# Kernel tuning notes

Measured on AMD Instinct MI355X. Metric: run time of the kernel, lower is better.

Reference implementation:

```python
import jax, jax.numpy as jnp
import numpy as np

B, N, D, R, NUM_HEADS, S = 8, 512, 256, 6, 3, 1000


def setup_inputs() -> dict:
    key = jax.random.key(0)
    ks = jax.random.split(key, 12)
    init = lambda k, shape: jax.random.normal(k, shape, jnp.float32) * 0.02
    return {
        "symbol_ids": jax.random.randint(ks[0], (B, N), 0, S),
        "positions": jax.random.normal(ks[1], (B, N, 2), jnp.float32),
        "sym_table": init(ks[2], (S, D)),
        "layer_table": init(ks[3], (S, D)),      # layer-0 interpretation embedding
        "rel_W": init(ks[4], (R, D, D)),          # per-relation Linear weights (in,out)
        "rel_b": init(ks[5], (R, D)),
        "h1_W": init(ks[6], (NUM_HEADS, D, D)),   # interpretation head Linear1
        "h1_b": init(ks[7], (NUM_HEADS, D)),
        "h2_W": init(ks[8], (NUM_HEADS, D)),      # interpretation head Linear2 (D->1)
        "h2_b": init(ks[9], (NUM_HEADS,)),
        "out_W": init(ks[10], (D, D)),
        "out_b": init(ks[11], (D,)),
    }


def _relation_type(dx, dy):
    # Vectorized version of PositionalGrammar._get_relation_type (if/elif chain)
    return jnp.select(
        [dy > 0.5, dy < -0.5, dx < -0.5, dx > 0.5,
         (jnp.abs(dx) < 0.3) & (jnp.abs(dy) < 0.3)],
        [0, 1, 2, 3, 4], 5)


def _positional_grammar(symbols, positions, rel_W, rel_b):
    # transformed[b,j] = symbols[b,j] + sum_{i!=j} (symbols[b,i] @ W_r(i,j) + b_r(i,j))
    dx = positions[:, None, :, 0] - positions[:, :, None, 0]  # [b,i,j]
    dy = positions[:, None, :, 1] - positions[:, :, None, 1]
    rel = _relation_type(dx, dy)                               # [b,i,j] int
    n = symbols.shape[1]
    not_self = ~jnp.eye(n, dtype=bool)
    # one-hot relation mask, self-pairs excluded: [b,i,j,r]
    M = ((rel[..., None] == jnp.arange(R)) & not_self[None, :, :, None]).astype(symbols.dtype)
    T = jnp.einsum('bid,rde->brie', symbols, rel_W)            # per-relation transform of sources
    contrib = jnp.einsum('bijr,brie->bje', M, T)               # scatter-add over sources i
    bias = jnp.einsum('bijr,re->bje', M, rel_b)                # per-pair bias accumulation
    return symbols + contrib + bias


def reference(symbol_ids, positions, sym_table, layer_table, rel_W, rel_b,
              h1_W, h1_b, h2_W, h2_b, out_W, out_b):
    # SymbolEmbedding (calendar_pos=None path; layer=0)
    symbols = sym_table[symbol_ids] + layer_table[symbol_ids]  # [B,N,D]
    # PositionalGrammar
    symbols = _positional_grammar(symbols, positions, rel_W, rel_b)
    # LayeredInterpretation: 3 heads of Linear-GELU-Linear(D->1)
    h = jax.nn.gelu(jnp.einsum('bnd,rde->brne', symbols, h1_W)
                    + h1_b[None, :, None, :], approximate=False)
    interp = jnp.einsum('brne,re->brn', h, h2_W) + h2_b[None, :, None]  # [B,3,N]
    # output projection
    output = symbols @ out_W + out_b
    return (output,
            interp[:, 0, :, None],   # exoteric  [B,N,1]
            interp[:, 1, :, None],   # esoteric
            interp[:, 2, :, None],   # sacred
            symbols)
```

## Files before the change

kernel.cpp:

```cpp
#include <hip/hip_runtime.h>
#include <hip/hip_bf16.h>
#include <math.h>

#define BB 8
#define NN 512
#define DD 256
#define BNT 4096

typedef __attribute__((ext_vector_type(8))) short short8;
typedef __attribute__((ext_vector_type(4))) float f32x4;

#define OFF_S0T   0u
#define OFF_GC    524288u
#define OFF_WCT   3670016u
#define OFF_WBT   3866624u
#define OFF_BB    3997696u
#define OFF_CNT   3998720u
#define OFF_REL   4015104u

#define OUT0_OFF   0u
#define INTERP_OFF 1048576u
#define SYM_OFF    1060864u

__device__ __forceinline__ float gelu_exact(float x) {
    return 0.5f * x * (1.0f + erff(x * 0.70710678118654752f));
}

__device__ __forceinline__ ushort f2bf(float x) {
    __hip_bfloat16 h = __float2bfloat16(x);
    union { __hip_bfloat16 b; ushort u; } cv;
    cv.b = h;
    return cv.u;
}

typedef __attribute__((address_space(3))) unsigned int  lds_u32;
typedef __attribute__((address_space(1))) unsigned int  glb_u32;
__device__ __forceinline__ void gload16(const void* g, void* l) {
    __builtin_amdgcn_global_load_lds((const glb_u32*)g, (lds_u32*)l, 16, 0, 0);
}

__device__ __forceinline__ int rel_of(float dx, float dy) {
    int r = (fabsf(dx) < 0.3f && fabsf(dy) < 0.3f) ? 4 : 5;
    r = (dx >  0.5f) ? 3 : r;
    r = (dx < -0.5f) ? 2 : r;
    r = (dy < -0.5f) ? 1 : r;
    r = (dy >  0.5f) ? 0 : r;
    return r;
}

__device__ __forceinline__ short8 onehot8(uint2 cw, unsigned rr) {
    union { ushort u[8]; short8 v; } o;
    unsigned m = rr * 0x01010101u;
    unsigned x = cw.x ^ m, y = cw.y ^ m;
#pragma unroll
    for (int t = 0; t < 4; t++) {
        o.u[t]     = (((x >> (8 * t)) & 255u) == 0u) ? 0x3F80 : 0;
        o.u[t + 4] = (((y >> (8 * t)) & 255u) == 0u) ? 0x3F80 : 0;
    }
    return o.v;
}

__device__ __forceinline__ unsigned zbyte_mask(unsigned t) {
    return ~(((t & 0x7F7F7F7Fu) + 0x7F7F7F7Fu) | t) & 0x80808080u;
}

#define WAVE_IDS()                                             \
    const int lane = tid & 63, w = tid >> 6;                   \
    const int wm = w >> 1, wn = w & 1;                         \
    const int quad = lane >> 4, l15 = lane & 15;               \
    const int sm = tid >> 2, sq = tid & 3;                     \
    (void)sm; (void)sq;

#define ACC_INIT()                                             \
    f32x4 acc[2][2];                                           \
    _Pragma("unroll") for (int mt = 0; mt < 2; mt++)           \
    _Pragma("unroll") for (int nt = 0; nt < 2; nt++)           \
        acc[mt][nt] = (f32x4){0.f, 0.f, 0.f, 0.f};

#define MFMA4(a0, a1, b0, b1)                                                     \
    acc[0][0] = __builtin_amdgcn_mfma_f32_16x16x32_bf16(a0, b0, acc[0][0], 0, 0, 0); \
    acc[0][1] = __builtin_amdgcn_mfma_f32_16x16x32_bf16(a0, b1, acc[0][1], 0, 0, 0); \
    acc[1][0] = __builtin_amdgcn_mfma_f32_16x16x32_bf16(a1, b0, acc[1][0], 0, 0, 0); \
    acc[1][1] = __builtin_amdgcn_mfma_f32_16x16x32_bf16(a1, b1, acc[1][1], 0, 0, 0);

#define MFMA_STEP(Abuf, Bbuf)                                                \
    {                                                                        \
        short8 af[2], bfr[2];                                                \
        _Pragma("unroll")                                                    \
        for (int mt = 0; mt < 2; mt++)                                       \
            af[mt] = *(const short8*)&(Abuf)[(quad * 64 + wm * 32 + mt * 16 + l15) * 8]; \
        _Pragma("unroll")                                                    \
        for (int nt = 0; nt < 2; nt++)                                       \
            bfr[nt] = *(const short8*)&(Bbuf)[(quad * 64 + wn * 32 + nt * 16 + l15) * 8]; \
        MFMA4(af[0], af[1], bfr[0], bfr[1]);                                 \
    }

__global__ __launch_bounds__(256) void front_kernel(
    const int* __restrict__ ids, const float* __restrict__ positions,
    const float* __restrict__ symt, const float* __restrict__ layt,
    const float* __restrict__ relW, const float* __restrict__ h1W,
    const float* __restrict__ outW, const float* __restrict__ h1b,
    const float* __restrict__ outb, const float* __restrict__ h2b,
    ushort* __restrict__ WcT, ushort* __restrict__ WbT,
    float* __restrict__ bbig, float* __restrict__ outI,
    float* __restrict__ symOut, ushort* __restrict__ s0T,
    unsigned char* __restrict__ rel, ushort* __restrict__ cnts)
{
    __shared__ float shbuf[32 * 257];
    int blk = blockIdx.x, tid = threadIdx.x;
    if (blk < 1536) {
        int idx = blk * 256 + tid;
        {
            int e = idx / 1536, k = idx - e * 1536;
            int r = k >> 8, d = k & 255;
            WcT[idx] = f2bf(relW[(r * DD + d) * DD + e]);
        }
        if (idx < 262144) {
            int c = idx >> 8, d = idx & 255;
            float v;
            if (c < 768) { int r = c >> 8, e = c & 255; v = h1W[(r * DD + d) * DD + e]; }
            else         { v = outW[d * DD + (c - 768)]; }
            WbT[idx] = f2bf(v);
        }
        if (idx < 3 * BNT) outI[idx] = h2b[idx >> 12];
        if (idx < 1024) bbig[idx] = (idx < 768) ? h1b[idx] : outb[idx - 768];
    } else if (blk < 1664) {
        int row0 = (blk - 1536) * 32;
        int b = row0 >> 9, i0 = row0 & 511;
        int rl = tid >> 3, dq = (tid & 7) * 4;
        int row = row0 + rl;
        int id = ids[row];
#pragma unroll
        for (int u = 0; u < 8; u++) {
            int d = dq + u * 32;
            float4 a = *(const float4*)&symt[(size_t)id * DD + d];
            float4 c = *(const float4*)&layt[(size_t)id * DD + d];
            float4 v = {a.x + c.x, a.y + c.y, a.z + c.z, a.w + c.w};
            *(float4*)&symOut[(size_t)row * DD + d] = v;
            shbuf[rl * 257 + d + 0] = v.x;
            shbuf[rl * 257 + d + 1] = v.y;
            shbuf[rl * 257 + d + 2] = v.z;
            shbuf[rl * 257 + d + 3] = v.w;
        }
        __syncthreads();
        int dd = tid;
        union { ushort u[32]; uint4 q[4]; } pk;
#pragma unroll
        for (int ii = 0; ii < 32; ii++) pk.u[ii] = f2bf(shbuf[ii * 257 + dd]);
        ushort* dst = s0T + ((size_t)(b * DD + dd)) * 512 + i0;
#pragma unroll
        for (int q = 0; q < 4; q++) ((uint4*)dst)[q] = pk.q[q];
    } else {
        float* px = shbuf;
        float* py = shbuf + NN;
        int blk2 = blk - 1664;
        int b = blk2 >> 6;
        int j0 = (blk2 & 63) << 3;
        int jl = tid >> 5, sub = tid & 31;
        for (int i = tid; i < NN; i += 256) {
            float2 p = ((const float2*)positions)[b * NN + i];
            px[i] = p.x; py[i] = p.y;
        }
        __syncthreads();
        int j = j0 + jl;
        float xj = px[j], yj = py[j];
        union { unsigned char u8[16]; unsigned wd[4]; uint4 v; } codes;
#pragma unroll
        for (int t = 0; t < 16; t++) {
            int i = sub * 16 + t;
            int r = rel_of(xj - px[i], yj - py[i]);
            r = (i == j) ? 6 : r;
            codes.u8[t] = (unsigned char)r;
        }
        *(uint4*)&rel[((size_t)(b * NN + j)) * NN + sub * 16] = codes.v;
        int cnt[6];
#pragma unroll
        for (int r = 0; r < 6; r++) {
            unsigned m = (unsigned)r * 0x01010101u;
            int c = 0;
#pragma unroll
            for (int k = 0; k < 4; k++)
                c += __builtin_popcount(zbyte_mask(codes.wd[k] ^ m));
            cnt[r] = c;
        }
#pragma unroll
        for (int r = 0; r < 6; r++) {
            cnt[r] += __shfl_xor(cnt[r], 1);
            cnt[r] += __shfl_xor(cnt[r], 2);
            cnt[r] += __shfl_xor(cnt[r], 4);
            cnt[r] += __shfl_xor(cnt[r], 8);
            cnt[r] += __shfl_xor(cnt[r], 16);
        }
        if (sub == 0) {
            uint4 pq;
            pq.x = (unsigned)cnt[0] | ((unsigned)cnt[1] << 16);
            pq.y = (unsigned)cnt[2] | ((unsigned)cnt[3] << 16);
            pq.z = (unsigned)cnt[4] | ((unsigned)cnt[5] << 16);
            pq.w = 0u;
            *(uint4*)&cnts[((size_t)(b * NN + j)) * 8] = pq;
        }
    }
}

__global__ __launch_bounds__(256) void aggT_kernel(
    const unsigned char* __restrict__ rel, const ushort* __restrict__ s0T,
    ushort* __restrict__ Gc)
{
    __shared__ ushort Bls[2][4096];
    int tid = threadIdx.x;
    int z = blockIdx.z;
    int b = z / 6;
    unsigned rr = (unsigned)(z - b * 6);
    int row0 = blockIdx.y * 64;
    int col0 = blockIdx.x * 64;
    WAVE_IDS();
    ACC_INIT();
    const ushort* gB = s0T + ((size_t)(b * DD) + col0 + lane) * 512 + w * 8;
    const unsigned char* gC0 = rel + ((size_t)(b * NN) + row0 + wm * 32 + l15) * NN + quad * 8;
    const unsigned char* gC1 = gC0 + 16 * NN;

#define AGT_STAGE(s, buf)                                     \
    gload16(gB + (s) * 64,      &Bls[buf][ w      * 512]);    \
    gload16(gB + (s) * 64 + 32, &Bls[buf][(w + 4) * 512]);

    uint2 cc[2][2], cn[2][2];
    cc[0][0] = *(const uint2*)(gC0);
    cc[0][1] = *(const uint2*)(gC0 + 32);
    cc[1][0] = *(const uint2*)(gC1);
    cc[1][1] = *(const uint2*)(gC1 + 32);
    AGT_STAGE(0, 0);
    __syncthreads();
#pragma unroll
    for (int s = 0; s < 8; s++) {
        if (s < 7) {
            AGT_STAGE(s + 1, (s + 1) & 1);
            cn[0][0] = *(const uint2*)(gC0 + (s + 1) * 64);
            cn[0][1] = *(const uint2*)(gC0 + (s + 1) * 64 + 32);
            cn[1][0] = *(const uint2*)(gC1 + (s + 1) * 64);
            cn[1][1] = *(const uint2*)(gC1 + (s + 1) * 64 + 32);
        }
#pragma unroll
        for (int h = 0; h < 2; h++) {
            short8 a0 = onehot8(cc[0][h], rr);
            short8 a1 = onehot8(cc[1][h], rr);
            short8 b0 = *(const short8*)&Bls[s & 1][((h * 4 + quad) * 64 + wn * 32 + l15) * 8];
            short8 b1 = *(const short8*)&Bls[s & 1][((h * 4 + quad) * 64 + wn * 32 + 16 + l15) * 8];
            MFMA4(a0, a1, b0, b1);
        }
        if (s < 7) {
            cc[0][0] = cn[0][0]; cc[0][1] = cn[0][1];
            cc[1][0] = cn[1][0]; cc[1][1] = cn[1][1];
        }
        __syncthreads();
    }
#undef AGT_STAGE
#pragma unroll
    for (int mt = 0; mt < 2; mt++)
#pragma unroll
        for (int nt = 0; nt < 2; nt++)
#pragma unroll
            for (int v = 0; v < 4; v++) {
                int j = row0 + wm * 32 + mt * 16 + quad * 4 + v;
                int d = col0 + wn * 32 + nt * 16 + l15;
                Gc[((size_t)(b * NN) + j) * 1536 + rr * 256 + d] =
                    f2bf(acc[mt][nt][v]);
            }
}

__global__ __launch_bounds__(256) void projC_kernel(
    const ushort* __restrict__ Gc, const ushort* __restrict__ WcT,
    const ushort* __restrict__ cnts, const float* __restrict__ relb,
    float* __restrict__ symOut)
{
    __shared__ ushort Als[2][8192], Bls[2][8192];
    int tid = threadIdx.x;
    int row0 = blockIdx.y * 64;
    int col0 = blockIdx.x * 64;
    WAVE_IDS();
    ACC_INIT();
    const ushort* gA = Gc  + (size_t)(row0 + lane) * 1536 + w * 8;
    const ushort* gB = WcT + (size_t)(col0 + lane) * 1536 + w * 8;

#define PJ_STAGE(s, buf)                                                    \
    _Pragma("unroll")                                                       \
    for (int p = 0; p < 4; p++) {                                           \
        gload16(gA + (s) * 128 + p * 32, &Als[buf][(w + p * 4) * 512]);     \
        gload16(gB + (s) * 128 + p * 32, &Bls[buf][(w + p * 4) * 512]);     \
    }

    PJ_STAGE(0, 0);
    __syncthreads();
#pragma unroll
    for (int s = 0; s < 12; s++) {
        if (s < 11) { PJ_STAGE(s + 1, (s + 1) & 1); }
#pragma unroll
        for (int h = 0; h < 4; h++) {
            short8 a0 = *(const short8*)&Als[s & 1][((h * 4 + quad) * 64 + wm * 32 + l15) * 8];
            short8 a1 = *(const short8*)&Als[s & 1][((h * 4 + quad) * 64 + wm * 32 + 16 + l15) * 8];
            short8 b0 = *(const short8*)&Bls[s & 1][((h * 4 + quad) * 64 + wn * 32 + l15) * 8];
            short8 b1 = *(const short8*)&Bls[s & 1][((h * 4 + quad) * 64 + wn * 32 + 16 + l15) * 8];
            MFMA4(a0, a1, b0, b1);
        }
        __syncthreads();
    }
#undef PJ_STAGE
#pragma unroll
    for (int mt = 0; mt < 2; mt++)
#pragma unroll
        for (int v = 0; v < 4; v++) {
            int row = row0 + wm * 32 + mt * 16 + quad * 4 + v;
            const ushort* cp = &cnts[(size_t)row * 8];
            float c0 = cp[0], c1 = cp[1], c2 = cp[2];
            float c3 = cp[3], c4 = cp[4], c5 = cp[5];
#pragma unroll
            for (int nt = 0; nt < 2; nt++) {
                int e = col0 + wn * 32 + nt * 16 + l15;
                float bias = c0 * relb[e]            + c1 * relb[DD + e]
                           + c2 * relb[2 * DD + e]   + c3 * relb[3 * DD + e]
                           + c4 * relb[4 * DD + e]   + c5 * relb[5 * DD + e];
                float* po = &symOut[(size_t)row * DD + e];
                *po = *po + acc[mt][nt][v] + bias;
            }
        }
}

__global__ __launch_bounds__(256) void gemm2_kernel(
    const float* __restrict__ symOut, const ushort* __restrict__ WbT,
    const float* __restrict__ bbig, const float* __restrict__ h2W,
    float* __restrict__ out0, float* __restrict__ outI)
{
    __shared__ ushort Als[2][2048], Bls[2][2048];
    int tid = threadIdx.x;
    int row0 = blockIdx.y * 64, col0 = blockIdx.x * 64;
    WAVE_IDS();
    ACC_INIT();
    const float*  gA = symOut + (size_t)(row0 + sm) * DD + sq * 8;
    const ushort* gB = WbT + (size_t)(col0 + lane) * DD + w * 8;
    const int lo = (sq * 64 + sm) * 8;

#define G2_STAGE(a0, a1, buf)                                       \
    {                                                               \
        union alignas(16) { ushort u[8]; uint4 v; } am;             \
        am.u[0] = f2bf(a0.x); am.u[1] = f2bf(a0.y);                 \
        am.u[2] = f2bf(a0.z); am.u[3] = f2bf(a0.w);                 \
        am.u[4] = f2bf(a1.x); am.u[5] = f2bf(a1.y);                 \
        am.u[6] = f2bf(a1.z); am.u[7] = f2bf(a1.w);                 \
        *(uint4*)&Als[buf][lo] = am.v;                              \
    }

    float4 a0 = *(const float4*)gA;
    float4 a1 = *(const float4*)(gA + 4);
    gload16(gB, &Bls[0][w * 512]);
    G2_STAGE(a0, a1, 0);
    __syncthreads();
#pragma unroll
    for (int s = 0; s < 8; s++) {
        float4 x = a0, y = a1;
        if (s < 7) {
            x = *(const float4*)(gA + (s + 1) * 32);
            y = *(const float4*)(gA + (s + 1) * 32 + 4);
            gload16(gB + (s + 1) * 32, &Bls[(s + 1) & 1][w * 512]);
        }
        MFMA_STEP(Als[s & 1], Bls[s & 1]);
        if (s < 7) { G2_STAGE(x, y, (s + 1) & 1); }
        __syncthreads();
    }
#undef G2_STAGE
    if (col0 >= 768) {
#pragma unroll
        for (int nt = 0; nt < 2; nt++) {
            int c = col0 + wn * 32 + nt * 16 + l15;
            float bb = bbig[c];
#pragma unroll
            for (int mt = 0; mt < 2; mt++)
#pragma unroll
                for (int v = 0; v < 4; v++) {
                    int row = row0 + wm * 32 + mt * 16 + quad * 4 + v;
                    out0[(size_t)row * DD + (c - 768)] = acc[mt][nt][v] + bb;
                }
        }
    } else {
        int head = col0 >> 8;
        float part[2][4];
#pragma unroll
        for (int mt = 0; mt < 2; mt++)
#pragma unroll
            for (int v = 0; v < 4; v++) part[mt][v] = 0.f;
#pragma unroll
        for (int nt = 0; nt < 2; nt++) {
            int c = col0 + wn * 32 + nt * 16 + l15;
            float bb = bbig[c];
            float w2 = h2W[c];
#pragma unroll
            for (int mt = 0; mt < 2; mt++)
#pragma unroll
                for (int v = 0; v < 4; v++)
                    part[mt][v] += gelu_exact(acc[mt][nt][v] + bb) * w2;
        }
#pragma unroll
        for (int mt = 0; mt < 2; mt++)
#pragma unroll
            for (int v = 0; v < 4; v++) {
                float p = part[mt][v];
                p += __shfl_xor(p, 1); p += __shfl_xor(p, 2);
                p += __shfl_xor(p, 4); p += __shfl_xor(p, 8);
                if (l15 == 0) {
                    int row = row0 + wm * 32 + mt * 16 + quad * 4 + v;
                    atomicAdd(&outI[head * BNT + row], p);
                }
            }
    }
}

extern "C" void kernel_launch(void* const* d_in, const int* in_sizes, int n_in,
                              void* d_out, int out_size, void* d_ws, size_t ws_size,
                              hipStream_t stream)
{
    const int*   ids  = (const int*)d_in[0];
    const float* pos  = (const float*)d_in[1];
    const float* symt = (const float*)d_in[2];
    const float* layt = (const float*)d_in[3];
    const float* relW = (const float*)d_in[4];
    const float* relb = (const float*)d_in[5];
    const float* h1W  = (const float*)d_in[6];
    const float* h1b  = (const float*)d_in[7];
    const float* h2W  = (const float*)d_in[8];
    const float* h2b  = (const float*)d_in[9];
    const float* outW = (const float*)d_in[10];
    const float* outb = (const float*)d_in[11];
    float* out = (float*)d_out;
    float* ws  = (float*)d_ws;

    ushort* s0T  = (ushort*)(ws + OFF_S0T);
    ushort* Gc   = (ushort*)(ws + OFF_GC);
    ushort* WcT  = (ushort*)(ws + OFF_WCT);
    ushort* WbT  = (ushort*)(ws + OFF_WBT);
    float*  bbig = ws + OFF_BB;
    ushort* cnts = (ushort*)(ws + OFF_CNT);
    unsigned char* rel = (unsigned char*)(ws + OFF_REL);

    front_kernel<<<2176, 256, 0, stream>>>(ids, pos, symt, layt, relW, h1W, outW,
                                           h1b, outb, h2b, WcT, WbT, bbig,
                                           out + INTERP_OFF, out + SYM_OFF, s0T,
                                           rel, cnts);
    aggT_kernel<<<dim3(4, 8, 48), 256, 0, stream>>>(rel, s0T, Gc);
    projC_kernel<<<dim3(4, 64), 256, 0, stream>>>(Gc, WcT, cnts, relb,
                                                  out + SYM_OFF);
    gemm2_kernel<<<dim3(16, 64), 256, 0, stream>>>(out + SYM_OFF, WbT,
                                                   bbig, h2W,
                                                   out + OUT0_OFF, out + INTERP_OFF);
}
```

Baseline: 163.0 us.

## Tile weight transposes through LDS and restructure GEMM kernels to preload B operands

The front kernel's weight transposes and bf16 conversions now go through 64x64 LDS tiles, so global reads and writes are coalesced, and the bias and interp initialisation stores are vectorised. This shrinks the grid from 2176 to 813 blocks. aggT and gemm2 now load the whole B tile into LDS once and read A operands straight from global memory into registers, which removes the per-step barriers. projC loads Gc fragments directly from global and double-buffers only the weight slabs, with three large stages. Per-block LDS use goes up and A reads become uncoalesced register loads, which may cost occupancy and bandwidth.

```diff
diff --git a/kernel.cpp b/kernel.cpp
--- a/kernel.cpp
+++ b/kernel.cpp
@@ -33,6 +33,13 @@
     return cv.u;
 }
 
+__device__ __forceinline__ short8 pack_bf8(float4 x, float4 y) {
+    union { ushort u[8]; short8 v; } o;
+    o.u[0] = f2bf(x.x); o.u[1] = f2bf(x.y); o.u[2] = f2bf(x.z); o.u[3] = f2bf(x.w);
+    o.u[4] = f2bf(y.x); o.u[5] = f2bf(y.y); o.u[6] = f2bf(y.z); o.u[7] = f2bf(y.w);
+    return o.v;
+}
+
 typedef __attribute__((address_space(3))) unsigned int  lds_u32;
 typedef __attribute__((address_space(1))) unsigned int  glb_u32;
 __device__ __forceinline__ void gload16(const void* g, void* l) {
@@ -67,9 +74,7 @@
 #define WAVE_IDS()                                             \
     const int lane = tid & 63, w = tid >> 6;                   \
     const int wm = w >> 1, wn = w & 1;                         \
-    const int quad = lane >> 4, l15 = lane & 15;               \
-    const int sm = tid >> 2, sq = tid & 3;                     \
-    (void)sm; (void)sq;
+    const int quad = lane >> 4, l15 = lane & 15;
 
 #define ACC_INIT()                                             \
     f32x4 acc[2][2];                                           \
@@ -83,17 +88,14 @@
     acc[1][0] = __builtin_amdgcn_mfma_f32_16x16x32_bf16(a1, b0, acc[1][0], 0, 0, 0); \
     acc[1][1] = __builtin_amdgcn_mfma_f32_16x16x32_bf16(a1, b1, acc[1][1], 0, 0, 0);
 
-#define MFMA_STEP(Abuf, Bbuf)                                                \
-    {                                                                        \
-        short8 af[2], bfr[2];                                                \
-        _Pragma("unroll")                                                    \
-        for (int mt = 0; mt < 2; mt++)                                       \
-            af[mt] = *(const short8*)&(Abuf)[(quad * 64 + wm * 32 + mt * 16 + l15) * 8]; \
-        _Pragma("unroll")                                                    \
-        for (int nt = 0; nt < 2; nt++)                                       \
-            bfr[nt] = *(const short8*)&(Bbuf)[(quad * 64 + wn * 32 + nt * 16 + l15) * 8]; \
-        MFMA4(af[0], af[1], bfr[0], bfr[1]);                                 \
-    }
+#define FB_WCT   0
+#define FB_H1    96
+#define FB_OUTW  144
+#define FB_OUTI  160
+#define FB_BB    172
+#define FB_GATH  173
+#define FB_CLS   301
+#define FB_TOTAL 813
 
 __global__ __launch_bounds__(256) void front_kernel(
     const int* __restrict__ ids, const float* __restrict__ positions,
@@ -108,24 +110,44 @@
 {
     __shared__ float shbuf[32 * 257];
     int blk = blockIdx.x, tid = threadIdx.x;
-    if (blk < 1536) {
-        int idx = blk * 256 + tid;
-        {
-            int e = idx / 1536, k = idx - e * 1536;
-            int r = k >> 8, d = k & 255;
-            WcT[idx] = f2bf(relW[(r * DD + d) * DD + e]);
-        }
-        if (idx < 262144) {
-            int c = idx >> 8, d = idx & 255;
-            float v;
-            if (c < 768) { int r = c >> 8, e = c & 255; v = h1W[(r * DD + d) * DD + e]; }
-            else         { v = outW[d * DD + (c - 768)]; }
-            WbT[idx] = f2bf(v);
-        }
-        if (idx < 3 * BNT) outI[idx] = h2b[idx >> 12];
-        if (idx < 1024) bbig[idx] = (idx < 768) ? h1b[idx] : outb[idx - 768];
-    } else if (blk < 1664) {
-        int row0 = (blk - 1536) * 32;
+    if (blk < FB_OUTI) {
+        int kl = tid & 63, g4 = tid >> 6;
+        const float* src; int srow, scol;
+        ushort* dst; int drow, dstride;
+        int dcol;
+        if (blk < FB_H1) {
+            int t = blk, rdt = t >> 2, et = t & 3;
+            src = relW; srow = rdt * 64; scol = et * 64;
+            dst = WcT; drow = et * 64; dstride = 1536; dcol = rdt * 64;
+        } else if (blk < FB_OUTW) {
+            int t = blk - FB_H1, r = t >> 4, dt = (t >> 2) & 3, et = t & 3;
+            src = h1W + (size_t)r * DD * DD; srow = dt * 64; scol = et * 64;
+            dst = WbT; drow = r * 256 + et * 64; dstride = 256; dcol = dt * 64;
+        } else {
+            int t = blk - FB_OUTW, dt = t >> 2, et = t & 3;
+            src = outW; srow = dt * 64; scol = et * 64;
+            dst = WbT; drow = 768 + et * 64; dstride = 256; dcol = dt * 64;
+        }
+#pragma unroll
+        for (int p = 0; p < 16; p++) {
+            int rl = p * 4 + g4;
+            shbuf[rl * 65 + kl] = src[(size_t)(srow + rl) * 256 + scol + kl];
+        }
+        __syncthreads();
+#pragma unroll
+        for (int q = 0; q < 16; q++) {
+            int el = q * 4 + g4;
+            dst[(size_t)(drow + el) * dstride + dcol + kl] = f2bf(shbuf[kl * 65 + el]);
+        }
+    } else if (blk < FB_BB) {
+        int idx = (blk - FB_OUTI) * 256 + tid;
+        float v = h2b[idx >> 10];
+        ((float4*)outI)[idx] = (float4){v, v, v, v};
+    } else if (blk < FB_GATH) {
+        ((float4*)bbig)[tid] = (tid < 192) ? ((const float4*)h1b)[tid]
+                                           : ((const float4*)outb)[tid - 192];
+    } else if (blk < FB_CLS) {
+        int row0 = (blk - FB_GATH) * 32;
         int b = row0 >> 9, i0 = row0 & 511;
         int rl = tid >> 3, dq = (tid & 7) * 4;
         int row = row0 + rl;
@@ -153,7 +175,7 @@
     } else {
         float* px = shbuf;
         float* py = shbuf + NN;
-        int blk2 = blk - 1664;
+        int blk2 = blk - FB_CLS;
         int b = blk2 >> 6;
         int j0 = (blk2 & 63) << 3;
         int jl = tid >> 5, sub = tid & 31;
@@ -206,7 +228,7 @@
     const unsigned char* __restrict__ rel, const ushort* __restrict__ s0T,
     ushort* __restrict__ Gc)
 {
-    __shared__ ushort Bls[2][4096];
+    __shared__ ushort Bls[64 * 512];
     int tid = threadIdx.x;
     int z = blockIdx.z;
     int b = z / 6;
@@ -215,45 +237,25 @@
     int col0 = blockIdx.x * 64;
     WAVE_IDS();
     ACC_INIT();
-    const ushort* gB = s0T + ((size_t)(b * DD) + col0 + lane) * 512 + w * 8;
+    const ushort* gB = s0T + ((size_t)(b * DD) + col0 + lane) * 512;
+#pragma unroll
+    for (int t = 0; t < 16; t++) {
+        int m = w * 16 + t;
+        gload16(gB + m * 8, &Bls[m * 512]);
+    }
     const unsigned char* gC0 = rel + ((size_t)(b * NN) + row0 + wm * 32 + l15) * NN + quad * 8;
     const unsigned char* gC1 = gC0 + 16 * NN;
-
-#define AGT_STAGE(s, buf)                                     \
-    gload16(gB + (s) * 64,      &Bls[buf][ w      * 512]);    \
-    gload16(gB + (s) * 64 + 32, &Bls[buf][(w + 4) * 512]);
-
-    uint2 cc[2][2], cn[2][2];
-    cc[0][0] = *(const uint2*)(gC0);
-    cc[0][1] = *(const uint2*)(gC0 + 32);
-    cc[1][0] = *(const uint2*)(gC1);
-    cc[1][1] = *(const uint2*)(gC1 + 32);
-    AGT_STAGE(0, 0);
     __syncthreads();
 #pragma unroll
-    for (int s = 0; s < 8; s++) {
-        if (s < 7) {
-            AGT_STAGE(s + 1, (s + 1) & 1);
-            cn[0][0] = *(const uint2*)(gC0 + (s + 1) * 64);
-            cn[0][1] = *(const uint2*)(gC0 + (s + 1) * 64 + 32);
-            cn[1][0] = *(const uint2*)(gC1 + (s + 1) * 64);
-            cn[1][1] = *(const uint2*)(gC1 + (s + 1) * 64 + 32);
-        }
-#pragma unroll
-        for (int h = 0; h < 2; h++) {
-            short8 a0 = onehot8(cc[0][h], rr);
-            short8 a1 = onehot8(cc[1][h], rr);
-            short8 b0 = *(const short8*)&Bls[s & 1][((h * 4 + quad) * 64 + wn * 32 + l15) * 8];
-            short8 b1 = *(const short8*)&Bls[s & 1][((h * 4 + quad) * 64 + wn * 32 + 16 + l15) * 8];
-            MFMA4(a0, a1, b0, b1);
-        }
-        if (s < 7) {
-            cc[0][0] = cn[0][0]; cc[0][1] = cn[0][1];
-            cc[1][0] = cn[1][0]; cc[1][1] = cn[1][1];
-        }
-        __syncthreads();
-    }
-#undef AGT_STAGE
+    for (int s = 0; s < 16; s++) {
+        uint2 c0 = *(const uint2*)(gC0 + s * 32);
+        uint2 c1 = *(const uint2*)(gC1 + s * 32);
+        short8 a0 = onehot8(c0, rr);
+        short8 a1 = onehot8(c1, rr);
+        short8 b0 = *(const short8*)&Bls[((s * 4 + quad) * 64 + wn * 32 + l15) * 8];
+        short8 b1 = *(const short8*)&Bls[((s * 4 + quad) * 64 + wn * 32 + 16 + l15) * 8];
+        MFMA4(a0, a1, b0, b1);
+    }
 #pragma unroll
     for (int mt = 0; mt < 2; mt++)
 #pragma unroll
@@ -272,38 +274,43 @@
     const ushort* __restrict__ cnts, const float* __restrict__ relb,
     float* __restrict__ symOut)
 {
-    __shared__ ushort Als[2][8192], Bls[2][8192];
+    __shared__ ushort Bls[2][64 * 512];
     int tid = threadIdx.x;
     int row0 = blockIdx.y * 64;
     int col0 = blockIdx.x * 64;
     WAVE_IDS();
     ACC_INIT();
-    const ushort* gA = Gc  + (size_t)(row0 + lane) * 1536 + w * 8;
-    const ushort* gB = WcT + (size_t)(col0 + lane) * 1536 + w * 8;
-
-#define PJ_STAGE(s, buf)                                                    \
-    _Pragma("unroll")                                                       \
-    for (int p = 0; p < 4; p++) {                                           \
-        gload16(gA + (s) * 128 + p * 32, &Als[buf][(w + p * 4) * 512]);     \
-        gload16(gB + (s) * 128 + p * 32, &Bls[buf][(w + p * 4) * 512]);     \
+    const ushort* gB  = WcT + (size_t)(col0 + lane) * 1536;
+    const ushort* gA0 = Gc + (size_t)(row0 + wm * 32 + l15) * 1536 + quad * 8;
+    const ushort* gA1 = gA0 + (size_t)16 * 1536;
+
+#define PJ_STAGE(zc, buf)                                         \
+    _Pragma("unroll")                                             \
+    for (int t = 0; t < 16; t++) {                                \
+        int m = w * 16 + t;                                       \
+        gload16(gB + (zc) * 512 + m * 8, &Bls[buf][m * 512]);     \
+    }
+#define PJ_COMPUTE(zc, buf)                                                       \
+    _Pragma("unroll")                                                             \
+    for (int s = 0; s < 16; s++) {                                                \
+        short8 a0 = *(const short8*)(gA0 + (zc) * 512 + s * 32);                  \
+        short8 a1 = *(const short8*)(gA1 + (zc) * 512 + s * 32);                  \
+        short8 b0 = *(const short8*)&Bls[buf][((s * 4 + quad) * 64 + wn * 32 + l15) * 8]; \
+        short8 b1 = *(const short8*)&Bls[buf][((s * 4 + quad) * 64 + wn * 32 + 16 + l15) * 8]; \
+        MFMA4(a0, a1, b0, b1);                                                    \
     }
 
     PJ_STAGE(0, 0);
     __syncthreads();
-#pragma unroll
-    for (int s = 0; s < 12; s++) {
-        if (s < 11) { PJ_STAGE(s + 1, (s + 1) & 1); }
-#pragma unroll
-        for (int h = 0; h < 4; h++) {
-            short8 a0 = *(const short8*)&Als[s & 1][((h * 4 + quad) * 64 + wm * 32 + l15) * 8];
-            short8 a1 = *(const short8*)&Als[s & 1][((h * 4 + quad) * 64 + wm * 32 + 16 + l15) * 8];
-            short8 b0 = *(const short8*)&Bls[s & 1][((h * 4 + quad) * 64 + wn * 32 + l15) * 8];
-            short8 b1 = *(const short8*)&Bls[s & 1][((h * 4 + quad) * 64 + wn * 32 + 16 + l15) * 8];
-            MFMA4(a0, a1, b0, b1);
-        }
-        __syncthreads();
-    }
+    PJ_STAGE(1, 1);
+    PJ_COMPUTE(0, 0);
+    __syncthreads();
+    PJ_STAGE(2, 0);
+    PJ_COMPUTE(1, 1);
+    __syncthreads();
+    PJ_COMPUTE(2, 0);
 #undef PJ_STAGE
+#undef PJ_COMPUTE
 #pragma unroll
     for (int mt = 0; mt < 2; mt++)
 #pragma unroll
@@ -329,43 +336,32 @@
     const float* __restrict__ bbig, const float* __restrict__ h2W,
     float* __restrict__ out0, float* __restrict__ outI)
 {
-    __shared__ ushort Als[2][2048], Bls[2][2048];
+    __shared__ ushort Bls[32 * 512];
     int tid = threadIdx.x;
     int row0 = blockIdx.y * 64, col0 = blockIdx.x * 64;
     WAVE_IDS();
     ACC_INIT();
-    const float*  gA = symOut + (size_t)(row0 + sm) * DD + sq * 8;
-    const ushort* gB = WbT + (size_t)(col0 + lane) * DD + w * 8;
-    const int lo = (sq * 64 + sm) * 8;
-
-#define G2_STAGE(a0, a1, buf)                                       \
-    {                                                               \
-        union alignas(16) { ushort u[8]; uint4 v; } am;             \
-        am.u[0] = f2bf(a0.x); am.u[1] = f2bf(a0.y);                 \
-        am.u[2] = f2bf(a0.z); am.u[3] = f2bf(a0.w);                 \
-        am.u[4] = f2bf(a1.x); am.u[5] = f2bf(a1.y);                 \
-        am.u[6] = f2bf(a1.z); am.u[7] = f2bf(a1.w);                 \
-        *(uint4*)&Als[buf][lo] = am.v;                              \
-    }
-
-    float4 a0 = *(const float4*)gA;
-    float4 a1 = *(const float4*)(gA + 4);
-    gload16(gB, &Bls[0][w * 512]);
-    G2_STAGE(a0, a1, 0);
+    const ushort* gB = WbT + (size_t)(col0 + lane) * 256;
+#pragma unroll
+    for (int t = 0; t < 8; t++) {
+        int m = w * 8 + t;
+        gload16(gB + m * 8, &Bls[m * 512]);
+    }
+    const float* gA0 = symOut + (size_t)(row0 + wm * 32 + l15) * 256 + quad * 8;
+    const float* gA1 = gA0 + 16 * 256;
     __syncthreads();
 #pragma unroll
     for (int s = 0; s < 8; s++) {
-        float4 x = a0, y = a1;
-        if (s < 7) {
-            x = *(const float4*)(gA + (s + 1) * 32);
-            y = *(const float4*)(gA + (s + 1) * 32 + 4);
-            gload16(gB + (s + 1) * 32, &Bls[(s + 1) & 1][w * 512]);
-        }
-        MFMA_STEP(Als[s & 1], Bls[s & 1]);
-        if (s < 7) { G2_STAGE(x, y, (s + 1) & 1); }
-        __syncthreads();
-    }
-#undef G2_STAGE
+        float4 x0 = *(const float4*)(gA0 + s * 32);
+        float4 y0 = *(const float4*)(gA0 + s * 32 + 4);
+        float4 x1 = *(const float4*)(gA1 + s * 32);
+        float4 y1 = *(const float4*)(gA1 + s * 32 + 4);
+        short8 a0 = pack_bf8(x0, y0);
+        short8 a1 = pack_bf8(x1, y1);
+        short8 b0 = *(const short8*)&Bls[((s * 4 + quad) * 64 + wn * 32 + l15) * 8];
+        short8 b1 = *(const short8*)&Bls[((s * 4 + quad) * 64 + wn * 32 + 16 + l15) * 8];
+        MFMA4(a0, a1, b0, b1);
+    }
     if (col0 >= 768) {
 #pragma unroll
         for (int nt = 0; nt < 2; nt++) {
@@ -439,10 +435,10 @@
     ushort* cnts = (ushort*)(ws + OFF_CNT);
     unsigned char* rel = (unsigned char*)(ws + OFF_REL);
 
-    front_kernel<<<2176, 256, 0, stream>>>(ids, pos, symt, layt, relW, h1W, outW,
-                                           h1b, outb, h2b, WcT, WbT, bbig,
-                                           out + INTERP_OFF, out + SYM_OFF, s0T,
-                                           rel, cnts);
+    front_kernel<<<FB_TOTAL, 256, 0, stream>>>(ids, pos, symt, layt, relW, h1W, outW,
+                                               h1b, outb, h2b, WcT, WbT, bbig,
+                                               out + INTERP_OFF, out + SYM_OFF, s0T,
+                                               rel, cnts);
     aggT_kernel<<<dim3(4, 8, 48), 256, 0, stream>>>(rel, s0T, Gc);
     projC_kernel<<<dim3(4, 64), 256, 0, stream>>>(Gc, WcT, cnts, relb,
                                                   out + SYM_OFF);
```

Result: slower. 176.8 us (+8.5%).
